# Kernel tuning notes

Measured on AMD Instinct MI355X. Metric: run time of the kernel, lower is better.

The kernel has to match this reference:

```python
import jax, jax.numpy as jnp
import numpy as np

BETA = 1.0  # init_kwargs beta

B, D, N = 8, 3, 4096
LATENT = 256

def setup_inputs() -> dict:
    key = jax.random.key(0)
    k1, k2, k3, k4 = jax.random.split(key, 4)
    return {
        "recon_x": jax.random.normal(k1, (B, D, N), dtype=jnp.float32),
        "x": jax.random.normal(k2, (B, D, N), dtype=jnp.float32),
        "mu": jax.random.normal(k3, (B, LATENT), dtype=jnp.float32),
        "logvar": jax.random.normal(k4, (B, LATENT), dtype=jnp.float32),
    }

def _chamfer(xc, yc):
    # xc, yc: [B, D, N] channels-first point clouds -> [B, N, D]
    xp = jnp.swapaxes(xc, 2, 1)  # [B, N, D]
    yp = jnp.swapaxes(yc, 2, 1)  # [B, M, D]
    # squared L2 pairwise distances via gram expansion (avoids [B,N,M,D] intermediate)
    x2 = jnp.sum(xp * xp, axis=-1)               # [B, N]
    y2 = jnp.sum(yp * yp, axis=-1)               # [B, M]
    xy = jnp.einsum("bnd,bmd->bnm", xp, yp)      # [B, N, M]
    dist = x2[:, :, None] + y2[:, None, :] - 2.0 * xy  # [B, N, M]
    min_x = jnp.min(dist, axis=2)  # [B, N] nearest y for each x
    min_y = jnp.min(dist, axis=1)  # [B, M] nearest x for each y
    return jnp.mean(min_x) + jnp.mean(min_y)

def _kl(mu, logvar):
    kld = -0.5 * jnp.sum(1.0 + logvar - mu * mu - jnp.exp(logvar))
    return kld / mu.shape[0]

def reference(recon_x, x, mu, logvar):
    recon_loss = _chamfer(recon_x, x)
    kld_loss = _kl(mu, logvar)
    total_loss = recon_loss + BETA * kld_loss
    return (total_loss, recon_loss, kld_loss)
```

## Files before the change

### kernel.cpp

```cpp
#include <hip/hip_runtime.h>
#include <math.h>

#define BB 8
#define DD 3
#define NN 4096
#define LATENT 256

#define Q 8
#define THREADS 256
#define QB (Q * THREADS)
#define QTILES (NN / QB)
#define BLOCKS_X (2 * BB * QTILES)
#define TOTQ (2 * BB * NN)

__global__ __launch_bounds__(THREADS)
void chamfer_stage1(const float* __restrict__ recon,
                    const float* __restrict__ x,
                    float* __restrict__ partial,
                    int C, int T)
{
    extern __shared__ float4 ly[];

    const int bx  = blockIdx.x;
    const int c   = blockIdx.y;
    const int dir = bx >> 4;
    const int rem = bx & 15;
    const int b   = rem >> 1;
    const int qt  = rem & 1;
    const int tid = threadIdx.x;

    const float* cloud = (dir ? recon : x) + (size_t)b * DD * NN;
    const float* query = (dir ? x : recon) + (size_t)b * DD * NN;

    for (int i = tid; i < T; i += THREADS) {
        int m = c * T + i;
        float y0 = cloud[0 * NN + m];
        float y1 = cloud[1 * NN + m];
        float y2 = cloud[2 * NN + m];
        ly[i] = make_float4(-2.0f * y0, -2.0f * y1, -2.0f * y2,
                            y0 * y0 + y1 * y1 + y2 * y2);
    }
    __syncthreads();

    float px[Q], py[Q], pz[Q], mn[Q];
    const int q0 = qt * QB + tid;
#pragma unroll
    for (int k = 0; k < Q; ++k) {
        int q = q0 + k * THREADS;
        px[k] = query[0 * NN + q];
        py[k] = query[1 * NN + q];
        pz[k] = query[2 * NN + q];
        mn[k] = 3.4e38f;
    }

#pragma unroll 4
    for (int m = 0; m < T; ++m) {
        float4 v = ly[m];
#pragma unroll
        for (int k = 0; k < Q; ++k) {
            float t = fmaf(px[k], v.x, fmaf(py[k], v.y, fmaf(pz[k], v.z, v.w)));
            mn[k] = fminf(mn[k], t);
        }
    }

    float* dst = partial + (size_t)c * TOTQ + (size_t)dir * (BB * NN) + b * NN + q0;
#pragma unroll
    for (int k = 0; k < Q; ++k) {
        float sx = px[k] * px[k] + py[k] * py[k] + pz[k] * pz[k];
        dst[k * THREADS] = sx + mn[k];
    }
}

__global__ __launch_bounds__(THREADS)
void chamfer_stage2(const float* __restrict__ partial,
                    float* __restrict__ sums, int C)
{
    __shared__ float red[4];
    const int tid = threadIdx.x;
    const int gq  = blockIdx.x * THREADS + tid;

    float m = partial[gq];
    for (int cc = 1; cc < C; ++cc)
        m = fminf(m, partial[(size_t)cc * TOTQ + gq]);

    for (int off = 32; off > 0; off >>= 1)
        m += __shfl_down(m, off);
    if ((tid & 63) == 0) red[tid >> 6] = m;
    __syncthreads();
    if (tid == 0)
        sums[blockIdx.x] = red[0] + red[1] + red[2] + red[3];
}

__global__ __launch_bounds__(THREADS)
void finalize_kernel(const float* __restrict__ sums,
                     const float* __restrict__ mu,
                     const float* __restrict__ logvar,
                     float* __restrict__ out)
{
    __shared__ float redA[4];
    __shared__ float redB[4];
    const int tid = threadIdx.x;

    float s = sums[tid];

    float kl = 0.0f;
    for (int i = tid; i < BB * LATENT; i += THREADS) {
        float m  = mu[i];
        float lv = logvar[i];
        kl += 1.0f + lv - m * m - expf(lv);
    }

    for (int off = 32; off > 0; off >>= 1) {
        s  += __shfl_down(s, off);
        kl += __shfl_down(kl, off);
    }
    if ((tid & 63) == 0) { redA[tid >> 6] = s; redB[tid >> 6] = kl; }
    __syncthreads();
    if (tid == 0) {
        float chamfer_sum = redA[0] + redA[1] + redA[2] + redA[3];
        float kl_sum      = redB[0] + redB[1] + redB[2] + redB[3];
        float recon = chamfer_sum / (float)(BB * NN);
        float kld   = -0.5f * kl_sum / (float)BB;
        out[0] = recon + kld;
        out[1] = recon;
        out[2] = kld;
    }
}

extern "C" void kernel_launch(void* const* d_in, const int* in_sizes, int n_in,
                              void* d_out, int out_size, void* d_ws, size_t ws_size,
                              hipStream_t stream)
{
    const float* recon  = (const float*)d_in[0];
    const float* x      = (const float*)d_in[1];
    const float* mu     = (const float*)d_in[2];
    const float* logvar = (const float*)d_in[3];
    float* out = (float*)d_out;

    int C = 1;
    for (int c = 16; c >= 1; c >>= 1) {
        size_t need = (size_t)c * TOTQ * sizeof(float) + 256 * sizeof(float);
        if (need <= ws_size) { C = c; break; }
    }
    const int T = NN / C;

    float* partial = (float*)d_ws;
    float* sums    = partial + (size_t)C * TOTQ;

    dim3 g1(BLOCKS_X, C);
    size_t lds = (size_t)T * sizeof(float4);
    chamfer_stage1<<<g1, THREADS, lds, stream>>>(recon, x, partial, C, T);
    chamfer_stage2<<<256, THREADS, 0, stream>>>(partial, sums, C);
    finalize_kernel<<<1, THREADS, 0, stream>>>(sums, mu, logvar, out);
}
```

Before: 35.31 us.

## Merge partial minima with atomicMin and fuse finalize via last-block pattern

Stage 1 no longer writes per-chunk partial minima. Each block now does an atomicMin on order-preserving uint-encoded floats into one slot array that a memset clears beforehand. The cloud split goes to 32 chunks and queries per thread drop to 4, giving many more blocks, and the inner loop prefetches two LDS points per iteration. Stage 2 reads the single minimum per query, and the last block to finish (found with an atomic counter) does the final KL and chamfer reduction, which removes the separate finalize launch. In exchange it adds atomic contention, a memset launch, and a counter reset inside stage 1 that relies on stream ordering.

```diff
diff --git a/kernel.cpp b/kernel.cpp
--- a/kernel.cpp
+++ b/kernel.cpp
@@ -2,106 +2,126 @@
 #include <math.h>
 
 #define BB 8
-#define DD 3
 #define NN 4096
 #define LATENT 256
 
-#define Q 8
 #define THREADS 256
+#define Q 4
 #define QB (Q * THREADS)
 #define QTILES (NN / QB)
 #define BLOCKS_X (2 * BB * QTILES)
-#define TOTQ (2 * BB * NN)
+#define CSPLIT 32
+#define TT (NN / CSPLIT)
+#define NSLOTS (2 * BB * NN)
 
-__global__ __launch_bounds__(THREADS)
+__device__ __forceinline__ unsigned enc(float f) {
+    unsigned b = __float_as_uint(f);
+    return (b & 0x80000000u) ? ~b : (b | 0x80000000u);
+}
+__device__ __forceinline__ float dec(unsigned k) {
+    unsigned b = (k & 0x80000000u) ? (k ^ 0x80000000u) : ~k;
+    return __uint_as_float(b);
+}
+
+__global__ __launch_bounds__(THREADS, 6)
 void chamfer_stage1(const float* __restrict__ recon,
                     const float* __restrict__ x,
-                    float* __restrict__ partial,
-                    int C, int T)
+                    unsigned* __restrict__ minkeys,
+                    unsigned* __restrict__ counter)
 {
-    extern __shared__ float4 ly[];
+    __shared__ float4 ly[TT];
 
     const int bx  = blockIdx.x;
     const int c   = blockIdx.y;
-    const int dir = bx >> 4;
-    const int rem = bx & 15;
-    const int b   = rem >> 1;
-    const int qt  = rem & 1;
+    const int dir = bx >> 5;
+    const int rem = bx & 31;
+    const int b   = rem >> 2;
+    const int qt  = rem & 3;
     const int tid = threadIdx.x;
 
-    const float* cloud = (dir ? recon : x) + (size_t)b * DD * NN;
-    const float* query = (dir ? x : recon) + (size_t)b * DD * NN;
+    if (bx == 0 && c == 0 && tid == 0) *counter = 0u;
 
-    for (int i = tid; i < T; i += THREADS) {
-        int m = c * T + i;
-        float y0 = cloud[0 * NN + m];
-        float y1 = cloud[1 * NN + m];
+    const float* cloud = (dir ? recon : x) + (size_t)b * 3 * NN;
+    const float* query = (dir ? x : recon) + (size_t)b * 3 * NN;
+
+    for (int i = tid; i < TT; i += THREADS) {
+        int m = c * TT + i;
+        float y0 = cloud[m];
+        float y1 = cloud[NN + m];
         float y2 = cloud[2 * NN + m];
         ly[i] = make_float4(-2.0f * y0, -2.0f * y1, -2.0f * y2,
                             y0 * y0 + y1 * y1 + y2 * y2);
     }
     __syncthreads();
 
+    const int q0 = qt * QB + tid;
     float px[Q], py[Q], pz[Q], mn[Q];
-    const int q0 = qt * QB + tid;
 #pragma unroll
     for (int k = 0; k < Q; ++k) {
         int q = q0 + k * THREADS;
-        px[k] = query[0 * NN + q];
-        py[k] = query[1 * NN + q];
+        px[k] = query[q];
+        py[k] = query[NN + q];
         pz[k] = query[2 * NN + q];
         mn[k] = 3.4e38f;
     }
 
+    float4 va = ly[0], vb = ly[1];
 #pragma unroll 4
-    for (int m = 0; m < T; ++m) {
-        float4 v = ly[m];
+    for (int m = 0; m < TT - 2; m += 2) {
+        float4 na = ly[m + 2];
+        float4 nb = ly[m + 3];
 #pragma unroll
         for (int k = 0; k < Q; ++k) {
-            float t = fmaf(px[k], v.x, fmaf(py[k], v.y, fmaf(pz[k], v.z, v.w)));
-            mn[k] = fminf(mn[k], t);
+            float t0 = fmaf(px[k], va.x, fmaf(py[k], va.y, fmaf(pz[k], va.z, va.w)));
+            float t1 = fmaf(px[k], vb.x, fmaf(py[k], vb.y, fmaf(pz[k], vb.z, vb.w)));
+            mn[k] = fminf(fminf(mn[k], t0), t1);
         }
+        va = na; vb = nb;
     }
-
-    float* dst = partial + (size_t)c * TOTQ + (size_t)dir * (BB * NN) + b * NN + q0;
 #pragma unroll
     for (int k = 0; k < Q; ++k) {
-        float sx = px[k] * px[k] + py[k] * py[k] + pz[k] * pz[k];
-        dst[k * THREADS] = sx + mn[k];
+        float t0 = fmaf(px[k], va.x, fmaf(py[k], va.y, fmaf(pz[k], va.z, va.w)));
+        float t1 = fmaf(px[k], vb.x, fmaf(py[k], vb.y, fmaf(pz[k], vb.z, vb.w)));
+        mn[k] = fminf(fminf(mn[k], t0), t1);
+        float sx  = fmaf(px[k], px[k], fmaf(py[k], py[k], pz[k] * pz[k]));
+        float val = sx + mn[k];
+        int slot  = dir * (BB * NN) + b * NN + q0 + k * THREADS;
+        atomicMin(&minkeys[slot], enc(val));
     }
 }
 
 __global__ __launch_bounds__(THREADS)
-void chamfer_stage2(const float* __restrict__ partial,
-                    float* __restrict__ sums, int C)
+void chamfer_stage2(const unsigned* __restrict__ minkeys,
+                    const float* __restrict__ mu,
+                    const float* __restrict__ logvar,
+                    float* __restrict__ sums,
+                    unsigned* __restrict__ counter,
+                    float* __restrict__ out)
 {
     __shared__ float red[4];
-    const int tid = threadIdx.x;
-    const int gq  = blockIdx.x * THREADS + tid;
-
-    float m = partial[gq];
-    for (int cc = 1; cc < C; ++cc)
-        m = fminf(m, partial[(size_t)cc * TOTQ + gq]);
-
-    for (int off = 32; off > 0; off >>= 1)
-        m += __shfl_down(m, off);
-    if ((tid & 63) == 0) red[tid >> 6] = m;
-    __syncthreads();
-    if (tid == 0)
-        sums[blockIdx.x] = red[0] + red[1] + red[2] + red[3];
-}
-
-__global__ __launch_bounds__(THREADS)
-void finalize_kernel(const float* __restrict__ sums,
-                     const float* __restrict__ mu,
-                     const float* __restrict__ logvar,
-                     float* __restrict__ out)
-{
     __shared__ float redA[4];
     __shared__ float redB[4];
+    __shared__ int amLast;
+
     const int tid = threadIdx.x;
+    const int bid = blockIdx.x;
 
-    float s = sums[tid];
+    float v = dec(minkeys[bid * THREADS + tid]);
+    for (int off = 32; off > 0; off >>= 1)
+        v += __shfl_down(v, off);
+    if ((tid & 63) == 0) red[tid >> 6] = v;
+    __syncthreads();
+
+    if (tid == 0) {
+        float tot = red[0] + red[1] + red[2] + red[3];
+        __hip_atomic_store(&sums[bid], tot, __ATOMIC_RELEASE, __HIP_MEMORY_SCOPE_AGENT);
+        unsigned old = __hip_atomic_fetch_add(counter, 1u, __ATOMIC_ACQ_REL, __HIP_MEMORY_SCOPE_AGENT);
+        amLast = (old == 255u);
+    }
+    __syncthreads();
+    if (!amLast) return;
+
+    float s = __hip_atomic_load(&sums[tid], __ATOMIC_ACQUIRE, __HIP_MEMORY_SCOPE_AGENT);
 
     float kl = 0.0f;
     for (int i = tid; i < BB * LATENT; i += THREADS) {
@@ -117,10 +137,8 @@
     if ((tid & 63) == 0) { redA[tid >> 6] = s; redB[tid >> 6] = kl; }
     __syncthreads();
     if (tid == 0) {
-        float chamfer_sum = redA[0] + redA[1] + redA[2] + redA[3];
-        float kl_sum      = redB[0] + redB[1] + redB[2] + redB[3];
-        float recon = chamfer_sum / (float)(BB * NN);
-        float kld   = -0.5f * kl_sum / (float)BB;
+        float recon = (redA[0] + redA[1] + redA[2] + redA[3]) / (float)(BB * NN);
+        float kld   = -0.5f * (redB[0] + redB[1] + redB[2] + redB[3]) / (float)BB;
         out[0] = recon + kld;
         out[1] = recon;
         out[2] = kld;
@@ -137,19 +155,14 @@
     const float* logvar = (const float*)d_in[3];
     float* out = (float*)d_out;
 
-    int C = 1;
-    for (int c = 16; c >= 1; c >>= 1) {
-        size_t need = (size_t)c * TOTQ * sizeof(float) + 256 * sizeof(float);
-        if (need <= ws_size) { C = c; break; }
-    }
-    const int T = NN / C;
+    unsigned* minkeys = (unsigned*)d_ws;
+    float*    sums    = (float*)(minkeys + NSLOTS);
+    unsigned* counter = (unsigned*)(sums + 256);
 
-    float* partial = (float*)d_ws;
-    float* sums    = partial + (size_t)C * TOTQ;
+    hipMemsetAsync(minkeys, 0xFF, (size_t)NSLOTS * sizeof(unsigned), stream);
 
-    dim3 g1(BLOCKS_X, C);
-    size_t lds = (size_t)T * sizeof(float4);
-    chamfer_stage1<<<g1, THREADS, lds, stream>>>(recon, x, partial, C, T);
-    chamfer_stage2<<<256, THREADS, 0, stream>>>(partial, sums, C);
-    finalize_kernel<<<1, THREADS, 0, stream>>>(sums, mu, logvar, out);
+    dim3 g1(BLOCKS_X, CSPLIT);
+    chamfer_stage1<<<g1, THREADS, 0, stream>>>(recon, x, minkeys, counter);
+    chamfer_stage2<<<NSLOTS / THREADS, THREADS, 0, stream>>>(minkeys, mu, logvar,
+                                                             sums, counter, out);
 }
```

After: 41.28 us. +16.9%, slower.
